# Performance work log

Measured on AMD Instinct MI355X. Metric: run time of the kernel, lower is better.

## Reference

```python
import jax, jax.numpy as jnp
import numpy as np

NEG_SLOPE = 0.01  # torch LeakyReLU default
VAR = 0.1


def _leaky(z):
    return jnp.where(z >= 0, z, NEG_SLOPE * z)


def _sconv(theta, bias, L, x):
    # theta: (C_out, C_in, 2), L: (M, M), x: (B, C_in, M)
    Lx = jnp.einsum('mn,bin->bim', L, x)                     # degree-1 Laplacian term
    y = jnp.einsum('oi,bim->bom', theta[:, :, 0], x) \
        + jnp.einsum('oi,bim->bom', theta[:, :, 1], Lx)
    if bias is not None:
        y = y + bias
    return y


def setup_inputs() -> dict:
    key = jax.random.key(0)
    ks = iter(jax.random.split(key, 32))
    B, Cin = 8, 4
    Ms = [2000, 6000, 4000]
    inp = {}
    for d, M in enumerate(Ms):
        inp[f'L{d}'] = jax.random.normal(next(ks), (M, M), jnp.float32) / np.sqrt(M)
        inp[f'x{d}'] = jax.random.normal(next(ks), (B, Cin, M), jnp.float32)
        inp[f'th{d}_1'] = VAR * jax.random.normal(next(ks), (16, 4, 2), jnp.float32)
        inp[f'b{d}_1'] = jnp.zeros((1, 16, 1), jnp.float32)
        inp[f'th{d}_2'] = VAR * jax.random.normal(next(ks), (32, 16, 2), jnp.float32)
    dims = [(96, 64), (64, 32), (32, 16), (16, 2)]
    for i, (din, dout) in enumerate(dims, start=1):
        bound = 1.0 / np.sqrt(din)
        inp[f'W{i}'] = jax.random.uniform(next(ks), (dout, din), jnp.float32, -bound, bound)
        inp[f'bb{i}'] = jax.random.uniform(next(ks), (dout,), jnp.float32, -bound, bound)
    return inp


def reference(L0, L1, L2, x0, x1, x2,
              th0_1, b0_1, th0_2,
              th1_1, b1_1, th1_2,
              th2_1, b2_1, th2_2,
              W1, bb1, W2, bb2, W3, bb3, W4, bb4):
    out0_1 = _sconv(th0_1, b0_1, L0, x0)
    out1_1 = _sconv(th1_1, b1_1, L1, x1)
    out2_1 = _sconv(th2_1, b2_1, L2, x2)
    out0_2 = _sconv(th0_2, None, L0, _leaky(out0_1))   # (B, 32, M0)
    out1_2 = _sconv(th1_2, None, L1, _leaky(out1_1))
    out2_2 = _sconv(th2_2, None, L2, _leaky(out2_1))
    # mean-pool over simplices, concat along channel dim -> (B, 96)
    pooled = jnp.concatenate([out0_2.mean(axis=2), out1_2.mean(axis=2), out2_2.mean(axis=2)], axis=1)
    h = pooled @ W1.T + bb1      # dropouts are identity at inference
    h = h @ W2.T + bb2
    h = h @ W3.T + bb3
    logits = h @ W4.T + bb4      # (B, 2)
    return (logits, out0_2, out1_2, out2_2)
```

## Files before the change

kernel.cpp:

```cpp
#include <hip/hip_runtime.h>
#include <stdint.h>

typedef __attribute__((ext_vector_type(4))) float f32x4;
typedef __attribute__((ext_vector_type(8))) __bf16 bf16x8;

constexpr int MS_[3] = {2000, 6000, 4000};
constexpr int MP_[3] = {2048, 6144, 4096};
constexpr int KS_[3] = {512, 1536, 1024};
constexpr int RB_[3] = {32, 96, 64};
constexpr int NB_[3] = {128, 384, 256};
constexpr int NTILE = 192;
constexpr int NGEMMB = 768;
constexpr long long OUT_OFF_[3] = {16, 512016, 2048016};

__device__ __forceinline__ unsigned short f2bf(float f) {
  __bf16 b = (__bf16)f;
  return *reinterpret_cast<unsigned short*>(&b);
}

__device__ __forceinline__ void gload_lds16(const void* g, void* l) {
  __builtin_amdgcn_global_load_lds(
      (const __attribute__((address_space(1))) unsigned int*)g,
      (__attribute__((address_space(3))) unsigned int*)l, 16, 0, 0);
}

template <int BN>
__device__ __forceinline__ void wait_main() {
  if constexpr (BN == 128) asm volatile("s_waitcnt vmcnt(12)" ::: "memory");
  else                     asm volatile("s_waitcnt vmcnt(6)" ::: "memory");
}
template <int BN>
__device__ __forceinline__ void wait_tail() {
  if constexpr (BN == 128) asm volatile("s_waitcnt vmcnt(8)" ::: "memory");
  else                     asm volatile("s_waitcnt vmcnt(5)" ::: "memory");
}
__device__ __forceinline__ void wait_zero() {
  asm volatile("s_waitcnt vmcnt(0)" ::: "memory");
}
__device__ __forceinline__ void bar_pin() {
  __builtin_amdgcn_s_barrier();
  __builtin_amdgcn_sched_barrier(0);
}

__device__ __forceinline__ void tile_decode(int bid, int& d, int& t) {
  if (bid < RB_[0]) { d = 0; t = bid; }
  else if (bid < RB_[0] + RB_[1]) { d = 1; t = bid - RB_[0]; }
  else { d = 2; t = bid - RB_[0] - RB_[1]; }
}

struct PrepArgs {
  const float* x[3];
  unsigned short* xT[3];
  float* zero0; int zero_n;
};

__global__ __launch_bounds__(256) void prep_k(PrepArgs pa) {
  int d, t; tile_decode(blockIdx.x, d, t);
  const int M = MS_[d], Mp = MP_[d];
  const float* x = pa.x[d];
  unsigned short* xT = pa.xT[d];
  const int tid = threadIdx.x;
  const int m0 = t * 64;
  const int ml = tid & 63, cg = tid >> 6;
  const int m = m0 + ml;
  const bool valid = m < M;
#pragma unroll
  for (int it = 0; it < 8; ++it) {
    int c = it * 4 + cg;
    float v = valid ? x[(size_t)c * M + m] : 0.f;
    xT[(size_t)c * Mp + m] = f2bf(v);
  }
  if (blockIdx.x == 0) {
    for (int i = tid; i < pa.zero_n; i += 256) pa.zero0[i] = 0.f;
  }
}

struct GemmArgs {
  const float* L[3];
  const unsigned short* B[3];
  float* P[3];
};

template <int BN>
__global__ __launch_bounds__(256, 2) void gemm_k(GemmArgs ga) {
  const int bid = blockIdx.x;
  int d, local;
  if (bid < NB_[1]) { d = 1; local = bid; }
  else if (bid < NB_[1] + NB_[2]) { d = 2; local = bid - NB_[1]; }
  else { d = 0; local = bid - NB_[1] - NB_[2]; }

  const int M = MS_[d], Mp = MP_[d], KS = KS_[d], RB = RB_[d];
  const int r = local % RB, s = local / RB;

  const float* __restrict__ Lp = ga.L[d];
  const unsigned short* __restrict__ Bt = ga.B[d];
  float* __restrict__ Pp = ga.P[d];

  const int m0 = r * 64;
  const int kt0 = s * KS;
  const int nsteps = KS >> 6;

  __shared__ __align__(16) unsigned short Bl[4][BN * 64];

  const int tid = threadIdx.x;
  const int lane = tid & 63;
  const int wave = tid >> 6;
  const int lr = lane & 15, lk = lane >> 4;
  constexpr int NR = BN / 16;
  constexpr int BI = BN / 32;

  int rowg = m0 + wave * 16 + lr;
  if (rowg > M - 1) rowg = M - 1;
  const float* __restrict__ pA = Lp + (size_t)rowg * M;

  const unsigned short* srcB[BI];
#pragma unroll
  for (int j = 0; j < BI; ++j) {
    int colg = (wave * BI + j) * 8 + (lane >> 3);
    int ke = ((lane & 7) * 8) ^ ((colg & 7) << 3);
    srcB[j] = Bt + (size_t)colg * Mp + ke;
  }

  f32x4 acc[NR];
#pragma unroll
  for (int n = 0; n < NR; ++n) acc[n] = (f32x4){0.f, 0.f, 0.f, 0.f};

  auto stageB = [&](int buf, int step) {
    const int kt = kt0 + step * 64;
#pragma unroll
    for (int j = 0; j < BI; ++j)
      gload_lds16(srcB[j] + kt, &Bl[buf][(wave * BI + j) * 512]);
  };
  auto loadA = [&](f32x4 (&ab)[2][2], int step) {
    const int kt = kt0 + step * 64;
#pragma unroll
    for (int kk = 0; kk < 2; ++kk) {
      int k = kt + kk * 32 + lk * 8;
      if (k + 8 > M) k = 0;
      const float* p = pA + k;
      ab[kk][0] = *reinterpret_cast<const f32x4*>(p);
      ab[kk][1] = *reinterpret_cast<const f32x4*>(p + 4);
    }
  };
  auto compute = [&](f32x4 (&ab)[2][2], int buf) {
    bf16x8 af[2];
#pragma unroll
    for (int kk = 0; kk < 2; ++kk)
#pragma unroll
      for (int j = 0; j < 4; ++j) {
        af[kk][j] = (__bf16)ab[kk][0][j];
        af[kk][4 + j] = (__bf16)ab[kk][1][j];
      }
    const unsigned short* Bb = &Bl[buf][0];
#pragma unroll
    for (int nr = 0; nr < NR; ++nr) {
      const int col = nr * 16 + lr;
      const int base = col * 64, swz = (col & 7) << 3;
      bf16x8 b0 = *reinterpret_cast<const bf16x8*>(&Bb[base + ((lk * 8) ^ swz)]);
      bf16x8 b1 = *reinterpret_cast<const bf16x8*>(&Bb[base + ((32 + lk * 8) ^ swz)]);
      acc[nr] = __builtin_amdgcn_mfma_f32_16x16x32_bf16(af[0], b0, acc[nr], 0, 0, 0);
      acc[nr] = __builtin_amdgcn_mfma_f32_16x16x32_bf16(af[1], b1, acc[nr], 0, 0, 0);
    }
  };

  f32x4 a0[2][2], a1[2][2];
  stageB(0, 0);
  loadA(a0, 0);
  stageB(1, 1);

  for (int t = 0; t < nsteps - 2; t += 2) {
    loadA(a1, t + 1);
    stageB((t + 2) & 3, t + 2);
    wait_main<BN>();
    bar_pin();
    compute(a0, t & 3);
    loadA(a0, t + 2);
    stageB((t + 3) & 3, t + 3);
    wait_main<BN>();
    bar_pin();
    compute(a1, (t + 1) & 3);
  }
  loadA(a1, nsteps - 1);
  wait_tail<BN>();
  bar_pin();
  compute(a0, (nsteps - 2) & 3);
  wait_zero();
  bar_pin();
  compute(a1, (nsteps - 1) & 3);

  const int rowb = m0 + wave * 16 + lk * 4;
#pragma unroll
  for (int nr = 0; nr < NR; ++nr) {
    const int cc = nr * 16 + lr;
#pragma unroll
    for (int j = 0; j < 4; ++j) {
      int rr = rowb + j;
      Pp[((size_t)s * Mp + rr) * BN + cc] = acc[nr][j];
    }
  }
}

struct EpiAArgs {
  const float* part1[3];
  const float* x[3];
  const float* th1[3];
  const float* b1[3];
  unsigned short* zT[3];
};

__global__ __launch_bounds__(256) void epiA_k(EpiAArgs ea) {
  int d, t; tile_decode(blockIdx.x, d, t);
  const int M = MS_[d], Mp = MP_[d];
  const int m0 = t * 64;
  __shared__ float Ys[32 * 66];
  __shared__ float Xs[32 * 66];
  const int tid = threadIdx.x;
  const float* part = ea.part1[d];
#pragma unroll
  for (int it = 0; it < 8; ++it) {
    int idx = it * 256 + tid;
    int m = idx >> 5, c = idx & 31;
    size_t base = (size_t)(m0 + m) * 32 + c;
    size_t st = (size_t)Mp * 32;
    float ssum = part[base] + part[st + base] + part[2 * st + base] + part[3 * st + base];
    Ys[c * 66 + m] = ssum;
  }
  {
    const float* x = ea.x[d];
    int m = tid & 63, cg = tid >> 6;
    bool valid = (m0 + m) < M;
#pragma unroll
    for (int it = 0; it < 8; ++it) {
      int c = it * 4 + cg;
      Xs[c * 66 + m] = valid ? x[(size_t)c * M + m0 + m] : 0.f;
    }
  }
  __syncthreads();
  const float* th = ea.th1[d];
  const float* bias = ea.b1[d];
  unsigned short* zT = ea.zT[d];
  const int m = tid & 63, cog = tid >> 6;
  const bool valid = (m0 + m) < M;
#pragma unroll
  for (int it = 0; it < 32; ++it) {
    int co = it * 4 + cog;
    int o = co & 15, b = co >> 4;
    float a = bias[o];
#pragma unroll
    for (int i = 0; i < 4; ++i) {
      int ci = b * 4 + i;
      a += th[(o * 4 + i) * 2] * Xs[ci * 66 + m] + th[(o * 4 + i) * 2 + 1] * Ys[ci * 66 + m];
    }
    float zz = (a >= 0.f) ? a : 0.01f * a;
    zT[(size_t)co * Mp + m0 + m] = valid ? f2bf(zz) : (unsigned short)0;
  }
}

struct EpiBArgs {
  const float* part2[3];
  const unsigned short* zT[3];
  const float* th2[3];
  float* out;
  float* csz;
  float* csy;
};

__global__ __launch_bounds__(256) void epiB_k(EpiBArgs eb) {
  int d, t; tile_decode(blockIdx.x, d, t);
  const int M = MS_[d], Mp = MP_[d];
  const int m0 = t * 64;
  __shared__ float Ys[128 * 66];
  __shared__ float red[256];
  const int tid = threadIdx.x;
  const float* part = eb.part2[d];
  float csum = 0.f;
#pragma unroll
  for (int it = 0; it < 32; ++it) {
    int idx = it * 256 + tid;
    int m = idx >> 7, c = idx & 127;
    size_t base = (size_t)(m0 + m) * 128 + c;
    size_t st = (size_t)Mp * 128;
    float ssum = part[base] + part[st + base] + part[2 * st + base] + part[3 * st + base];
    Ys[c * 66 + m] = ssum;
    if (m0 + m < M) csum += ssum;
  }
  red[tid] = csum;
  __syncthreads();
  if (tid < 128) atomicAdd(&eb.csy[d * 128 + tid], red[tid] + red[tid + 128]);

  const unsigned short* zT = eb.zT[d];
  const float* th = eb.th2[d];
  float* outp = eb.out + OUT_OFF_[d];
  const int m = tid & 63, g = tid >> 6;
  const bool valid = (m0 + m) < M;
#pragma unroll
  for (int bb = 0; bb < 2; ++bb) {
    int b = g * 2 + bb;
    float zv[16], yv[16];
#pragma unroll
    for (int o1 = 0; o1 < 16; ++o1) {
      int c = b * 16 + o1;
      unsigned short raw = zT[(size_t)c * Mp + m0 + m];
      __bf16 bf = *reinterpret_cast<__bf16*>(&raw);
      zv[o1] = (float)bf;
      yv[o1] = Ys[c * 66 + m];
    }
#pragma unroll
    for (int o1 = 0; o1 < 16; ++o1) {
      float v = zv[o1];
#pragma unroll
      for (int off = 32; off > 0; off >>= 1) v += __shfl_xor(v, off, 64);
      if (m == 0) atomicAdd(&eb.csz[d * 128 + b * 16 + o1], v);
    }
#pragma unroll
    for (int o2 = 0; o2 < 32; ++o2) {
      float v = 0.f;
#pragma unroll
      for (int o1 = 0; o1 < 16; ++o1)
        v += th[(o2 * 16 + o1) * 2] * zv[o1] + th[(o2 * 16 + o1) * 2 + 1] * yv[o1];
      if (valid) outp[(size_t)(b * 32 + o2) * M + m0 + m] = v;
    }
  }
}

struct MlpArgs {
  const float* csz; const float* csy;
  const float* th2[3];
  const float* W1; const float* b1;
  const float* W2; const float* b2;
  const float* W3; const float* b3;
  const float* W4; const float* b4;
  float* out;
};

__global__ __launch_bounds__(256) void mlp_k(MlpArgs ma) {
  __shared__ float pl[8][96];
  __shared__ float h1[8][64];
  __shared__ float h2[8][32];
  __shared__ float h3[8][16];
  const int tid = threadIdx.x;
  for (int id = tid; id < 768; id += 256) {
    int d = id >> 8, rem = id & 255, b = rem >> 5, o2 = rem & 31;
    const float* th = ma.th2[d];
    float invM = 1.f / (float)MS_[d];
    float v = 0.f;
    for (int o1 = 0; o1 < 16; ++o1)
      v += th[(o2 * 16 + o1) * 2] * ma.csz[d * 128 + b * 16 + o1] +
           th[(o2 * 16 + o1) * 2 + 1] * ma.csy[d * 128 + b * 16 + o1];
    pl[b][d * 32 + o2] = v * invM;
  }
  __syncthreads();
  for (int id = tid; id < 512; id += 256) {
    int b = id >> 6, j = id & 63;
    float v = ma.b1[j];
    for (int k = 0; k < 96; ++k) v += pl[b][k] * ma.W1[j * 96 + k];
    h1[b][j] = v;
  }
  __syncthreads();
  {
    int b = tid >> 5, j = tid & 31;
    float v = ma.b2[j];
    for (int k = 0; k < 64; ++k) v += h1[b][k] * ma.W2[j * 64 + k];
    h2[b][j] = v;
  }
  __syncthreads();
  if (tid < 128) {
    int b = tid >> 4, j = tid & 15;
    float v = ma.b3[j];
    for (int k = 0; k < 32; ++k) v += h2[b][k] * ma.W3[j * 32 + k];
    h3[b][j] = v;
  }
  __syncthreads();
  if (tid < 16) {
    int b = tid >> 1, j = tid & 1;
    float v = ma.b4[j];
    for (int k = 0; k < 16; ++k) v += h3[b][k] * ma.W4[j * 16 + k];
    ma.out[tid] = v;
  }
}

extern "C" void kernel_launch(void* const* d_in, const int* in_sizes, int n_in,
                              void* d_out, int out_size, void* d_ws, size_t ws_size,
                              hipStream_t stream) {
  (void)in_sizes; (void)n_in; (void)out_size; (void)ws_size;
  const float* L[3]   = {(const float*)d_in[0], (const float*)d_in[5], (const float*)d_in[10]};
  const float* x[3]   = {(const float*)d_in[1], (const float*)d_in[6], (const float*)d_in[11]};
  const float* th1[3] = {(const float*)d_in[2], (const float*)d_in[7], (const float*)d_in[12]};
  const float* b1[3]  = {(const float*)d_in[3], (const float*)d_in[8], (const float*)d_in[13]};
  const float* th2[3] = {(const float*)d_in[4], (const float*)d_in[9], (const float*)d_in[14]};
  const float* W1 = (const float*)d_in[15]; const float* bb1 = (const float*)d_in[16];
  const float* W2 = (const float*)d_in[17]; const float* bb2 = (const float*)d_in[18];
  const float* W3 = (const float*)d_in[19]; const float* bb3 = (const float*)d_in[20];
  const float* W4 = (const float*)d_in[21]; const float* bb4 = (const float*)d_in[22];
  float* out = (float*)d_out;

  char* ws = (char*)d_ws;
  size_t off = 0;
  auto alloc = [&](size_t bytes) {
    size_t r = off;
    off = (off + bytes + 255) & ~(size_t)255;
    return r;
  };
  const int MPs[3] = {2048, 6144, 4096};
  unsigned short* xT[3]; unsigned short* zT[3]; float* p1[3]; float* p2[3];
  for (int d = 0; d < 3; ++d) xT[d] = (unsigned short*)(ws + alloc((size_t)32 * MPs[d] * 2));
  for (int d = 0; d < 3; ++d) zT[d] = (unsigned short*)(ws + alloc((size_t)128 * MPs[d] * 2));
  for (int d = 0; d < 3; ++d) p1[d] = (float*)(ws + alloc((size_t)4 * MPs[d] * 32 * 4));
  for (int d = 0; d < 3; ++d) p2[d] = (float*)(ws + alloc((size_t)4 * MPs[d] * 128 * 4));
  float* csz = (float*)(ws + alloc((size_t)3 * 128 * 4));
  float* csy = (float*)(ws + alloc((size_t)3 * 128 * 4));

  PrepArgs pa;
  for (int d = 0; d < 3; ++d) { pa.x[d] = x[d]; pa.xT[d] = xT[d]; }
  pa.zero0 = csz; pa.zero_n = 768;
  prep_k<<<NTILE, 256, 0, stream>>>(pa);

  GemmArgs g1;
  for (int d = 0; d < 3; ++d) { g1.L[d] = L[d]; g1.B[d] = xT[d]; g1.P[d] = p1[d]; }
  gemm_k<32><<<NGEMMB, 256, 0, stream>>>(g1);

  EpiAArgs ea;
  for (int d = 0; d < 3; ++d) {
    ea.part1[d] = p1[d]; ea.x[d] = x[d]; ea.th1[d] = th1[d]; ea.b1[d] = b1[d]; ea.zT[d] = zT[d];
  }
  epiA_k<<<NTILE, 256, 0, stream>>>(ea);

  GemmArgs g2;
  for (int d = 0; d < 3; ++d) { g2.L[d] = L[d]; g2.B[d] = zT[d]; g2.P[d] = p2[d]; }
  gemm_k<128><<<NGEMMB, 256, 0, stream>>>(g2);

  EpiBArgs eb;
  for (int d = 0; d < 3; ++d) { eb.part2[d] = p2[d]; eb.zT[d] = zT[d]; eb.th2[d] = th2[d]; }
  eb.out = out; eb.csz = csz; eb.csy = csy;
  epiB_k<<<NTILE, 256, 0, stream>>>(eb);

  MlpArgs ma;
  ma.csz = csz; ma.csy = csy;
  for (int d = 0; d < 3; ++d) ma.th2[d] = th2[d];
  ma.W1 = W1; ma.b1 = bb1; ma.W2 = W2; ma.b2 = bb2;
  ma.W3 = W3; ma.b3 = bb3; ma.W4 = W4; ma.b4 = bb4;
  ma.out = out;
  mlp_k<<<1, 256, 0, stream>>>(ma);
}
```

Baseline: 187.5 us.

## Split GEMM into specialised kernels with wider split-K and retuned pipelines

The shared templated GEMM becomes two kernels. gemm1 (N=32) uses 128-row tiles with two M-fragments per wave and 16-way split-K, giving 1536 blocks at occupancy 4. gemm2 (N=128) moves to a 3-slot LDS ring at occupancy 3. Both get a unified steady-state loop with clamped prefetch in place of explicit tail handling. The goal is more parallelism and better latency hiding for the memory-bound L streaming of the first GEMM, at the cost of a 16-way partial reduction in epiA and a shared partial buffer reused by both stages.

```diff
diff --git a/kernel.cpp b/kernel.cpp
--- a/kernel.cpp
+++ b/kernel.cpp
@@ -6,11 +6,16 @@
 
 constexpr int MS_[3] = {2000, 6000, 4000};
 constexpr int MP_[3] = {2048, 6144, 4096};
-constexpr int KS_[3] = {512, 1536, 1024};
 constexpr int RB_[3] = {32, 96, 64};
-constexpr int NB_[3] = {128, 384, 256};
 constexpr int NTILE = 192;
-constexpr int NGEMMB = 768;
+constexpr int RBB1_[3] = {16, 48, 32};
+constexpr int NB1_[3] = {256, 768, 512};
+constexpr int NG1 = 1536;
+constexpr int KS1_[3] = {128, 384, 256};
+constexpr int RB2_[3] = {32, 96, 64};
+constexpr int NB2_[3] = {128, 384, 256};
+constexpr int NG2 = 768;
+constexpr int KS2_[3] = {512, 1536, 1024};
 constexpr long long OUT_OFF_[3] = {16, 512016, 2048016};
 
 __device__ __forceinline__ unsigned short f2bf(float f) {
@@ -24,19 +29,6 @@
       (__attribute__((address_space(3))) unsigned int*)l, 16, 0, 0);
 }
 
-template <int BN>
-__device__ __forceinline__ void wait_main() {
-  if constexpr (BN == 128) asm volatile("s_waitcnt vmcnt(12)" ::: "memory");
-  else                     asm volatile("s_waitcnt vmcnt(6)" ::: "memory");
-}
-template <int BN>
-__device__ __forceinline__ void wait_tail() {
-  if constexpr (BN == 128) asm volatile("s_waitcnt vmcnt(8)" ::: "memory");
-  else                     asm volatile("s_waitcnt vmcnt(5)" ::: "memory");
-}
-__device__ __forceinline__ void wait_zero() {
-  asm volatile("s_waitcnt vmcnt(0)" ::: "memory");
-}
 __device__ __forceinline__ void bar_pin() {
   __builtin_amdgcn_s_barrier();
   __builtin_amdgcn_sched_barrier(0);
@@ -75,61 +67,182 @@
   }
 }
 
-struct GemmArgs {
+struct G1Args {
   const float* L[3];
   const unsigned short* B[3];
   float* P[3];
 };
 
-template <int BN>
-__global__ __launch_bounds__(256, 2) void gemm_k(GemmArgs ga) {
+__global__ __launch_bounds__(256, 4) void gemm1_k(G1Args ga) {
   const int bid = blockIdx.x;
   int d, local;
-  if (bid < NB_[1]) { d = 1; local = bid; }
-  else if (bid < NB_[1] + NB_[2]) { d = 2; local = bid - NB_[1]; }
-  else { d = 0; local = bid - NB_[1] - NB_[2]; }
-
-  const int M = MS_[d], Mp = MP_[d], KS = KS_[d], RB = RB_[d];
+  if (bid < NB1_[1]) { d = 1; local = bid; }
+  else if (bid < NB1_[1] + NB1_[2]) { d = 2; local = bid - NB1_[1]; }
+  else { d = 0; local = bid - NB1_[1] - NB1_[2]; }
+
+  const int M = MS_[d], Mp = MP_[d], KS = KS1_[d], RB = RBB1_[d];
   const int r = local % RB, s = local / RB;
-
   const float* __restrict__ Lp = ga.L[d];
   const unsigned short* __restrict__ Bt = ga.B[d];
   float* __restrict__ Pp = ga.P[d];
 
-  const int m0 = r * 64;
+  const int m0 = r * 128;
   const int kt0 = s * KS;
-  const int nsteps = KS >> 6;
-
-  __shared__ __align__(16) unsigned short Bl[4][BN * 64];
+  const int ns = KS >> 6;
+
+  __shared__ __align__(16) unsigned short Bl[4][32 * 64];
 
   const int tid = threadIdx.x;
   const int lane = tid & 63;
   const int wave = tid >> 6;
   const int lr = lane & 15, lk = lane >> 4;
-  constexpr int NR = BN / 16;
-  constexpr int BI = BN / 32;
+
+  const float* pA[2];
+#pragma unroll
+  for (int mr = 0; mr < 2; ++mr) {
+    int row = m0 + wave * 32 + mr * 16 + lr;
+    if (row > M - 1) row = M - 1;
+    pA[mr] = Lp + (size_t)row * M;
+  }
+  const int colg = tid >> 3;
+  const int ke = ((tid & 7) * 8) ^ ((colg & 7) << 3);
+  const unsigned short* srcB = Bt + (size_t)colg * Mp + ke;
+
+  f32x4 acc[2][2];
+#pragma unroll
+  for (int a = 0; a < 2; ++a)
+#pragma unroll
+    for (int b = 0; b < 2; ++b) acc[a][b] = (f32x4){0.f, 0.f, 0.f, 0.f};
+
+  auto mstep = [&](int x) { return x < ns ? x : ns - 1; };
+  auto stageB = [&](int slot, int step) {
+    gload_lds16(srcB + kt0 + step * 64, &Bl[slot][tid * 8]);
+  };
+  auto loadA = [&](f32x4 (&ab)[2][2][2], int step) {
+    const int kt = kt0 + step * 64;
+#pragma unroll
+    for (int mr = 0; mr < 2; ++mr)
+#pragma unroll
+      for (int kk = 0; kk < 2; ++kk) {
+        int k = kt + kk * 32 + lk * 8;
+        if (k + 8 > M) k = 0;
+        const float* p = pA[mr] + k;
+        ab[mr][kk][0] = *reinterpret_cast<const f32x4*>(p);
+        ab[mr][kk][1] = *reinterpret_cast<const f32x4*>(p + 4);
+      }
+  };
+  auto compute = [&](f32x4 (&ab)[2][2][2], int slot) {
+    bf16x8 af[2][2];
+#pragma unroll
+    for (int mr = 0; mr < 2; ++mr)
+#pragma unroll
+      for (int kk = 0; kk < 2; ++kk)
+#pragma unroll
+        for (int j = 0; j < 4; ++j) {
+          af[mr][kk][j] = (__bf16)ab[mr][kk][0][j];
+          af[mr][kk][4 + j] = (__bf16)ab[mr][kk][1][j];
+        }
+    const unsigned short* Bb = &Bl[slot][0];
+#pragma unroll
+    for (int nr = 0; nr < 2; ++nr) {
+      const int col = nr * 16 + lr;
+      const int base = col * 64, swz = (col & 7) << 3;
+      bf16x8 b0 = *reinterpret_cast<const bf16x8*>(&Bb[base + ((lk * 8) ^ swz)]);
+      bf16x8 b1 = *reinterpret_cast<const bf16x8*>(&Bb[base + ((32 + lk * 8) ^ swz)]);
+#pragma unroll
+      for (int mr = 0; mr < 2; ++mr) {
+        acc[mr][nr] = __builtin_amdgcn_mfma_f32_16x16x32_bf16(af[mr][0], b0, acc[mr][nr], 0, 0, 0);
+        acc[mr][nr] = __builtin_amdgcn_mfma_f32_16x16x32_bf16(af[mr][1], b1, acc[mr][nr], 0, 0, 0);
+      }
+    }
+  };
+
+  f32x4 a0[2][2][2], a1[2][2][2];
+  stageB(0, 0);
+  stageB(2, mstep(2));
+  loadA(a0, 0);
+  stageB(1, mstep(1));
+  loadA(a1, mstep(1));
+
+  for (int t = 0; t < ns; t += 2) {
+    asm volatile("s_waitcnt vmcnt(9)" ::: "memory");
+    bar_pin();
+    stageB((t + 3) & 3, mstep(t + 3));
+    compute(a0, t & 3);
+    loadA(a0, mstep(t + 2));
+
+    asm volatile("s_waitcnt vmcnt(9)" ::: "memory");
+    bar_pin();
+    stageB((t + 4) & 3, mstep(t + 4));
+    compute(a1, (t + 1) & 3);
+    loadA(a1, mstep(t + 3));
+  }
+
+#pragma unroll
+  for (int mr = 0; mr < 2; ++mr) {
+    const int rowb = m0 + wave * 32 + mr * 16 + lk * 4;
+#pragma unroll
+    for (int nr = 0; nr < 2; ++nr) {
+      const int cc = nr * 16 + lr;
+#pragma unroll
+      for (int j = 0; j < 4; ++j)
+        Pp[((size_t)s * Mp + rowb + j) * 32 + cc] = acc[mr][nr][j];
+    }
+  }
+}
+
+struct G2Args {
+  const float* L[3];
+  const unsigned short* B[3];
+  float* P[3];
+};
+
+__global__ __launch_bounds__(256, 3) void gemm2_k(G2Args ga) {
+  const int bid = blockIdx.x;
+  int d, local;
+  if (bid < NB2_[1]) { d = 1; local = bid; }
+  else if (bid < NB2_[1] + NB2_[2]) { d = 2; local = bid - NB2_[1]; }
+  else { d = 0; local = bid - NB2_[1] - NB2_[2]; }
+
+  const int M = MS_[d], Mp = MP_[d], KS = KS2_[d], RB = RB2_[d];
+  const int r = local % RB, s = local / RB;
+  const float* __restrict__ Lp = ga.L[d];
+  const unsigned short* __restrict__ Bt = ga.B[d];
+  float* __restrict__ Pp = ga.P[d];
+
+  const int m0 = r * 64;
+  const int kt0 = s * KS;
+  const int ns = KS >> 6;
+
+  __shared__ __align__(16) unsigned short Bl[3][128 * 64];
+
+  const int tid = threadIdx.x;
+  const int lane = tid & 63;
+  const int wave = tid >> 6;
+  const int lr = lane & 15, lk = lane >> 4;
 
   int rowg = m0 + wave * 16 + lr;
   if (rowg > M - 1) rowg = M - 1;
   const float* __restrict__ pA = Lp + (size_t)rowg * M;
 
-  const unsigned short* srcB[BI];
-#pragma unroll
-  for (int j = 0; j < BI; ++j) {
-    int colg = (wave * BI + j) * 8 + (lane >> 3);
-    int ke = ((lane & 7) * 8) ^ ((colg & 7) << 3);
-    srcB[j] = Bt + (size_t)colg * Mp + ke;
-  }
-
-  f32x4 acc[NR];
-#pragma unroll
-  for (int n = 0; n < NR; ++n) acc[n] = (f32x4){0.f, 0.f, 0.f, 0.f};
-
-  auto stageB = [&](int buf, int step) {
+  const unsigned short* srcB[4];
+#pragma unroll
+  for (int j = 0; j < 4; ++j) {
+    int colg = (wave * 4 + j) * 8 + (lane >> 3);
+    int ke2 = ((lane & 7) * 8) ^ ((colg & 7) << 3);
+    srcB[j] = Bt + (size_t)colg * Mp + ke2;
+  }
+
+  f32x4 acc[8];
+#pragma unroll
+  for (int n = 0; n < 8; ++n) acc[n] = (f32x4){0.f, 0.f, 0.f, 0.f};
+
+  auto mstep = [&](int x) { return x < ns ? x : ns - 1; };
+  auto stageB = [&](int slot, int step) {
     const int kt = kt0 + step * 64;
 #pragma unroll
-    for (int j = 0; j < BI; ++j)
-      gload_lds16(srcB[j] + kt, &Bl[buf][(wave * BI + j) * 512]);
+    for (int j = 0; j < 4; ++j)
+      gload_lds16(srcB[j] + kt, &Bl[slot][(wave * 4 + j) * 512 + lane * 8]);
   };
   auto loadA = [&](f32x4 (&ab)[2][2], int step) {
     const int kt = kt0 + step * 64;
@@ -142,7 +255,7 @@
       ab[kk][1] = *reinterpret_cast<const f32x4*>(p + 4);
     }
   };
-  auto compute = [&](f32x4 (&ab)[2][2], int buf) {
+  auto compute = [&](f32x4 (&ab)[2][2], int slot) {
     bf16x8 af[2];
 #pragma unroll
     for (int kk = 0; kk < 2; ++kk)
@@ -151,9 +264,9 @@
         af[kk][j] = (__bf16)ab[kk][0][j];
         af[kk][4 + j] = (__bf16)ab[kk][1][j];
       }
-    const unsigned short* Bb = &Bl[buf][0];
-#pragma unroll
-    for (int nr = 0; nr < NR; ++nr) {
+    const unsigned short* Bb = &Bl[slot][0];
+#pragma unroll
+    for (int nr = 0; nr < 8; ++nr) {
       const int col = nr * 16 + lr;
       const int base = col * 64, swz = (col & 7) << 3;
       bf16x8 b0 = *reinterpret_cast<const bf16x8*>(&Bb[base + ((lk * 8) ^ swz)]);
@@ -166,37 +279,30 @@
   f32x4 a0[2][2], a1[2][2];
   stageB(0, 0);
   loadA(a0, 0);
-  stageB(1, 1);
-
-  for (int t = 0; t < nsteps - 2; t += 2) {
-    loadA(a1, t + 1);
-    stageB((t + 2) & 3, t + 2);
-    wait_main<BN>();
+  stageB(1, mstep(1));
+  loadA(a1, mstep(1));
+
+  for (int t = 0; t < ns; t += 2) {
+    asm volatile("s_waitcnt vmcnt(8)" ::: "memory");
     bar_pin();
-    compute(a0, t & 3);
-    loadA(a0, t + 2);
-    stageB((t + 3) & 3, t + 3);
-    wait_main<BN>();
+    stageB((t + 2) % 3, mstep(t + 2));
+    compute(a0, t % 3);
+    loadA(a0, mstep(t + 2));
+
+    asm volatile("s_waitcnt vmcnt(8)" ::: "memory");
     bar_pin();
-    compute(a1, (t + 1) & 3);
-  }
-  loadA(a1, nsteps - 1);
-  wait_tail<BN>();
-  bar_pin();
-  compute(a0, (nsteps - 2) & 3);
-  wait_zero();
-  bar_pin();
-  compute(a1, (nsteps - 1) & 3);
+    stageB((t + 3) % 3, mstep(t + 3));
+    compute(a1, (t + 1) % 3);
+    loadA(a1, mstep(t + 3));
+  }
 
   const int rowb = m0 + wave * 16 + lk * 4;
 #pragma unroll
-  for (int nr = 0; nr < NR; ++nr) {
+  for (int nr = 0; nr < 8; ++nr) {
     const int cc = nr * 16 + lr;
 #pragma unroll
-    for (int j = 0; j < 4; ++j) {
-      int rr = rowb + j;
-      Pp[((size_t)s * Mp + rr) * BN + cc] = acc[nr][j];
-    }
+    for (int j = 0; j < 4; ++j)
+      Pp[((size_t)s * Mp + rowb + j) * 128 + cc] = acc[nr][j];
   }
 }
 
@@ -216,13 +322,15 @@
   __shared__ float Xs[32 * 66];
   const int tid = threadIdx.x;
   const float* part = ea.part1[d];
+  const size_t st = (size_t)Mp * 32;
 #pragma unroll
   for (int it = 0; it < 8; ++it) {
     int idx = it * 256 + tid;
     int m = idx >> 5, c = idx & 31;
     size_t base = (size_t)(m0 + m) * 32 + c;
-    size_t st = (size_t)Mp * 32;
-    float ssum = part[base] + part[st + base] + part[2 * st + base] + part[3 * st + base];
+    float ssum = 0.f;
+#pragma unroll
+    for (int s5 = 0; s5 < 16; ++s5) ssum += part[s5 * st + base];
     Ys[c * 66 + m] = ssum;
   }
   {
@@ -402,11 +510,10 @@
     return r;
   };
   const int MPs[3] = {2048, 6144, 4096};
-  unsigned short* xT[3]; unsigned short* zT[3]; float* p1[3]; float* p2[3];
+  unsigned short* xT[3]; unsigned short* zT[3]; float* pb[3];
   for (int d = 0; d < 3; ++d) xT[d] = (unsigned short*)(ws + alloc((size_t)32 * MPs[d] * 2));
   for (int d = 0; d < 3; ++d) zT[d] = (unsigned short*)(ws + alloc((size_t)128 * MPs[d] * 2));
-  for (int d = 0; d < 3; ++d) p1[d] = (float*)(ws + alloc((size_t)4 * MPs[d] * 32 * 4));
-  for (int d = 0; d < 3; ++d) p2[d] = (float*)(ws + alloc((size_t)4 * MPs[d] * 128 * 4));
+  for (int d = 0; d < 3; ++d) pb[d] = (float*)(ws + alloc((size_t)16 * MPs[d] * 32 * 4));
   float* csz = (float*)(ws + alloc((size_t)3 * 128 * 4));
   float* csy = (float*)(ws + alloc((size_t)3 * 128 * 4));
 
@@ -415,22 +522,22 @@
   pa.zero0 = csz; pa.zero_n = 768;
   prep_k<<<NTILE, 256, 0, stream>>>(pa);
 
-  GemmArgs g1;
-  for (int d = 0; d < 3; ++d) { g1.L[d] = L[d]; g1.B[d] = xT[d]; g1.P[d] = p1[d]; }
-  gemm_k<32><<<NGEMMB, 256, 0, stream>>>(g1);
+  G1Args g1;
+  for (int d = 0; d < 3; ++d) { g1.L[d] = L[d]; g1.B[d] = xT[d]; g1.P[d] = pb[d]; }
+  gemm1_k<<<NG1, 256, 0, stream>>>(g1);
 
   EpiAArgs ea;
   for (int d = 0; d < 3; ++d) {
-    ea.part1[d] = p1[d]; ea.x[d] = x[d]; ea.th1[d] = th1[d]; ea.b1[d] = b1[d]; ea.zT[d] = zT[d];
+    ea.part1[d] = pb[d]; ea.x[d] = x[d]; ea.th1[d] = th1[d]; ea.b1[d] = b1[d]; ea.zT[d] = zT[d];
   }
   epiA_k<<<NTILE, 256, 0, stream>>>(ea);
 
-  GemmArgs g2;
-  for (int d = 0; d < 3; ++d) { g2.L[d] = L[d]; g2.B[d] = zT[d]; g2.P[d] = p2[d]; }
-  gemm_k<128><<<NGEMMB, 256, 0, stream>>>(g2);
+  G2Args g2;
+  for (int d = 0; d < 3; ++d) { g2.L[d] = L[d]; g2.B[d] = zT[d]; g2.P[d] = pb[d]; }
+  gemm2_k<<<NG2, 256, 0, stream>>>(g2);
 
   EpiBArgs eb;
-  for (int d = 0; d < 3; ++d) { eb.part2[d] = p2[d]; eb.zT[d] = zT[d]; eb.th2[d] = th2[d]; }
+  for (int d = 0; d < 3; ++d) { eb.part2[d] = pb[d]; eb.zT[d] = zT[d]; eb.th2[d] = th2[d]; }
   eb.out = out; eb.csz = csz; eb.csy = csy;
   epiB_k<<<NTILE, 256, 0, stream>>>(eb);
 
```

Measured after the change: 190.6 us. About the same (+1.6%).

## Stage L tiles through LDS ring, raise split-K for pass 1, split N for pass 2

Applied to the files above, without the earlier changes.

Both GEMM passes now load the fp32 L tile asynchronously into a swizzled LDS ring with global_load_lds instead of into registers, and use a single-step ring pipeline with a fixed vmcnt wait. Pass 1 uses a much larger split-K (8-16 splits) to get more blocks in flight. Pass 2 splits the 128 output columns into two 64-wide halves, doubling the blocks. This targets latency hiding and occupancy on the memory-bound L stream, at the cost of reading L twice in pass 2, more partial sums for epiA to reduce, and a shared partial buffer reused between passes.

```diff
diff --git a/kernel.cpp b/kernel.cpp
--- a/kernel.cpp
+++ b/kernel.cpp
@@ -6,12 +6,15 @@
 
 constexpr int MS_[3] = {2000, 6000, 4000};
 constexpr int MP_[3] = {2048, 6144, 4096};
-constexpr int KS_[3] = {512, 1536, 1024};
 constexpr int RB_[3] = {32, 96, 64};
-constexpr int NB_[3] = {128, 384, 256};
 constexpr int NTILE = 192;
-constexpr int NGEMMB = 768;
 constexpr long long OUT_OFF_[3] = {16, 512016, 2048016};
+
+constexpr int S1_[3] = {8, 16, 16};
+constexpr int KS1_[3] = {256, 384, 256};
+constexpr int NG1 = 1536 + 1024 + 256;
+constexpr int KS2_[3] = {512, 1536, 1024};
+constexpr int NG2 = 768 + 512 + 256;
 
 __device__ __forceinline__ unsigned short f2bf(float f) {
   __bf16 b = (__bf16)f;
@@ -24,19 +27,6 @@
       (__attribute__((address_space(3))) unsigned int*)l, 16, 0, 0);
 }
 
-template <int BN>
-__device__ __forceinline__ void wait_main() {
-  if constexpr (BN == 128) asm volatile("s_waitcnt vmcnt(12)" ::: "memory");
-  else                     asm volatile("s_waitcnt vmcnt(6)" ::: "memory");
-}
-template <int BN>
-__device__ __forceinline__ void wait_tail() {
-  if constexpr (BN == 128) asm volatile("s_waitcnt vmcnt(8)" ::: "memory");
-  else                     asm volatile("s_waitcnt vmcnt(5)" ::: "memory");
-}
-__device__ __forceinline__ void wait_zero() {
-  asm volatile("s_waitcnt vmcnt(0)" ::: "memory");
-}
 __device__ __forceinline__ void bar_pin() {
   __builtin_amdgcn_s_barrier();
   __builtin_amdgcn_sched_barrier(0);
@@ -75,22 +65,33 @@
   }
 }
 
-struct GemmArgs {
+struct GArgs {
   const float* L[3];
   const unsigned short* B[3];
   float* P[3];
 };
 
-template <int BN>
-__global__ __launch_bounds__(256, 2) void gemm_k(GemmArgs ga) {
-  const int bid = blockIdx.x;
-  int d, local;
-  if (bid < NB_[1]) { d = 1; local = bid; }
-  else if (bid < NB_[1] + NB_[2]) { d = 2; local = bid - NB_[1]; }
-  else { d = 0; local = bid - NB_[1] - NB_[2]; }
-
-  const int M = MS_[d], Mp = MP_[d], KS = KS_[d], RB = RB_[d];
-  const int r = local % RB, s = local / RB;
+template <int PASS>
+__global__ __launch_bounds__(256, 2) void gemm_k(GArgs ga) {
+  int bid = blockIdx.x;
+  int d, r, s, nh = 0;
+  if constexpr (PASS == 1) {
+    if (bid < 1536) { d = 1; r = bid % 96; s = bid / 96; }
+    else if (bid < 2560) { bid -= 1536; d = 2; r = bid % 64; s = bid / 64; }
+    else { bid -= 2560; d = 0; r = bid % 32; s = bid / 32; }
+  } else {
+    if (bid < 768) { d = 1; r = bid % 96; int q = bid / 96; nh = q & 1; s = q >> 1; }
+    else if (bid < 1280) { bid -= 768; d = 2; r = bid % 64; int q = bid / 64; nh = q & 1; s = q >> 1; }
+    else { bid -= 1280; d = 0; r = bid % 32; int q = bid / 32; nh = q & 1; s = q >> 1; }
+  }
+  const int M = MS_[d], Mp = MP_[d];
+  const int KS = (PASS == 1) ? KS1_[d] : KS2_[d];
+  const int ns = KS >> 6;
+  constexpr int BN = (PASS == 1) ? 32 : 64;
+  constexpr int PW = (PASS == 1) ? 32 : 128;
+  constexpr int RING = (PASS == 1) ? 4 : 3;
+  constexpr int NR = BN / 16;
+  constexpr int BI = BN / 32;
 
   const float* __restrict__ Lp = ga.L[d];
   const unsigned short* __restrict__ Bt = ga.B[d];
@@ -98,105 +99,101 @@
 
   const int m0 = r * 64;
   const int kt0 = s * KS;
-  const int nsteps = KS >> 6;
-
-  __shared__ __align__(16) unsigned short Bl[4][BN * 64];
+
+  __shared__ __align__(16) char Al[RING][64 * 256];
+  __shared__ __align__(16) char Bl[RING][BN * 128];
 
   const int tid = threadIdx.x;
   const int lane = tid & 63;
   const int wave = tid >> 6;
   const int lr = lane & 15, lk = lane >> 4;
-  constexpr int NR = BN / 16;
-  constexpr int BI = BN / 32;
-
-  int rowg = m0 + wave * 16 + lr;
-  if (rowg > M - 1) rowg = M - 1;
-  const float* __restrict__ pA = Lp + (size_t)rowg * M;
-
+
+  const float* pAsrc[4];
+  int koffA[4];
+#pragma unroll
+  for (int j = 0; j < 4; ++j) {
+    int ldsb = j * 4096 + tid * 16;
+    int row = ldsb >> 8;
+    int inner = (ldsb & 255) ^ ((row & 7) << 5);
+    int grow = m0 + row;
+    if (grow > M - 1) grow = M - 1;
+    pAsrc[j] = Lp + (size_t)grow * M;
+    koffA[j] = inner >> 2;
+  }
   const unsigned short* srcB[BI];
 #pragma unroll
   for (int j = 0; j < BI; ++j) {
-    int colg = (wave * BI + j) * 8 + (lane >> 3);
-    int ke = ((lane & 7) * 8) ^ ((colg & 7) << 3);
-    srcB[j] = Bt + (size_t)colg * Mp + ke;
+    int ldsb = j * 4096 + tid * 16;
+    int col = ldsb >> 7;
+    int inner = (ldsb & 127) ^ ((col & 7) << 4);
+    srcB[j] = Bt + (size_t)(nh * 64 + col) * Mp + (inner >> 1);
   }
 
   f32x4 acc[NR];
 #pragma unroll
   for (int n = 0; n < NR; ++n) acc[n] = (f32x4){0.f, 0.f, 0.f, 0.f};
 
-  auto stageB = [&](int buf, int step) {
+  auto mstep = [&](int x) { return x < ns ? x : ns - 1; };
+  auto stage = [&](int slot, int step) {
     const int kt = kt0 + step * 64;
 #pragma unroll
+    for (int j = 0; j < 4; ++j) {
+      int gk = kt + koffA[j];
+      if (gk + 4 > M) gk = 0;
+      gload_lds16(pAsrc[j] + gk, &Al[slot][j * 4096 + tid * 16]);
+    }
+#pragma unroll
     for (int j = 0; j < BI; ++j)
-      gload_lds16(srcB[j] + kt, &Bl[buf][(wave * BI + j) * 512]);
+      gload_lds16(srcB[j] + kt, &Bl[slot][j * 4096 + tid * 16]);
   };
-  auto loadA = [&](f32x4 (&ab)[2][2], int step) {
-    const int kt = kt0 + step * 64;
+  auto compute = [&](int slot) {
+    const char* Ab = &Al[slot][0];
+    const char* Bb = &Bl[slot][0];
+    const int rowl = wave * 16 + lr;
+    const int abase = rowl * 256;
+    const int aswz = (rowl & 7) << 5;
+    bf16x8 af[2];
 #pragma unroll
     for (int kk = 0; kk < 2; ++kk) {
-      int k = kt + kk * 32 + lk * 8;
-      if (k + 8 > M) k = 0;
-      const float* p = pA + k;
-      ab[kk][0] = *reinterpret_cast<const f32x4*>(p);
-      ab[kk][1] = *reinterpret_cast<const f32x4*>(p + 4);
-    }
-  };
-  auto compute = [&](f32x4 (&ab)[2][2], int buf) {
-    bf16x8 af[2];
-#pragma unroll
-    for (int kk = 0; kk < 2; ++kk)
+      int off = abase + ((kk * 128 + lk * 32) ^ aswz);
+      f32x4 v0 = *reinterpret_cast<const f32x4*>(Ab + off);
+      f32x4 v1 = *reinterpret_cast<const f32x4*>(Ab + off + 16);
 #pragma unroll
       for (int j = 0; j < 4; ++j) {
-        af[kk][j] = (__bf16)ab[kk][0][j];
-        af[kk][4 + j] = (__bf16)ab[kk][1][j];
+        af[kk][j] = (__bf16)v0[j];
+        af[kk][4 + j] = (__bf16)v1[j];
       }
-    const unsigned short* Bb = &Bl[buf][0];
+    }
 #pragma unroll
     for (int nr = 0; nr < NR; ++nr) {
       const int col = nr * 16 + lr;
-      const int base = col * 64, swz = (col & 7) << 3;
-      bf16x8 b0 = *reinterpret_cast<const bf16x8*>(&Bb[base + ((lk * 8) ^ swz)]);
-      bf16x8 b1 = *reinterpret_cast<const bf16x8*>(&Bb[base + ((32 + lk * 8) ^ swz)]);
+      const int bbase = col * 128, bswz = (col & 7) << 4;
+      bf16x8 b0 = *reinterpret_cast<const bf16x8*>(Bb + bbase + ((lk * 16) ^ bswz));
+      bf16x8 b1 = *reinterpret_cast<const bf16x8*>(Bb + bbase + ((64 + lk * 16) ^ bswz));
       acc[nr] = __builtin_amdgcn_mfma_f32_16x16x32_bf16(af[0], b0, acc[nr], 0, 0, 0);
       acc[nr] = __builtin_amdgcn_mfma_f32_16x16x32_bf16(af[1], b1, acc[nr], 0, 0, 0);
     }
   };
 
-  f32x4 a0[2][2], a1[2][2];
-  stageB(0, 0);
-  loadA(a0, 0);
-  stageB(1, 1);
-
-  for (int t = 0; t < nsteps - 2; t += 2) {
-    loadA(a1, t + 1);
-    stageB((t + 2) & 3, t + 2);
-    wait_main<BN>();
+  stage(0, 0);
+  stage(1, mstep(1));
+  if constexpr (RING == 4) stage(2, mstep(2));
+
+  for (int t = 0; t < ns; ++t) {
+    if constexpr (PASS == 1) asm volatile("s_waitcnt vmcnt(10)" ::: "memory");
+    else                     asm volatile("s_waitcnt vmcnt(6)" ::: "memory");
     bar_pin();
-    compute(a0, t & 3);
-    loadA(a0, t + 2);
-    stageB((t + 3) & 3, t + 3);
-    wait_main<BN>();
-    bar_pin();
-    compute(a1, (t + 1) & 3);
-  }
-  loadA(a1, nsteps - 1);
-  wait_tail<BN>();
-  bar_pin();
-  compute(a0, (nsteps - 2) & 3);
-  wait_zero();
-  bar_pin();
-  compute(a1, (nsteps - 1) & 3);
+    stage((t + RING - 1) % RING, mstep(t + RING - 1));
+    compute(t % RING);
+  }
 
   const int rowb = m0 + wave * 16 + lk * 4;
 #pragma unroll
   for (int nr = 0; nr < NR; ++nr) {
-    const int cc = nr * 16 + lr;
-#pragma unroll
-    for (int j = 0; j < 4; ++j) {
-      int rr = rowb + j;
-      Pp[((size_t)s * Mp + rr) * BN + cc] = acc[nr][j];
-    }
+    const int cc = (PASS == 1 ? 0 : nh * 64) + nr * 16 + lr;
+#pragma unroll
+    for (int j = 0; j < 4; ++j)
+      Pp[((size_t)s * Mp + rowb + j) * PW + cc] = acc[nr][j];
   }
 }
 
@@ -216,13 +213,15 @@
   __shared__ float Xs[32 * 66];
   const int tid = threadIdx.x;
   const float* part = ea.part1[d];
+  const size_t st = (size_t)Mp * 32;
+  const int S1 = S1_[d];
 #pragma unroll
   for (int it = 0; it < 8; ++it) {
     int idx = it * 256 + tid;
     int m = idx >> 5, c = idx & 31;
     size_t base = (size_t)(m0 + m) * 32 + c;
-    size_t st = (size_t)Mp * 32;
-    float ssum = part[base] + part[st + base] + part[2 * st + base] + part[3 * st + base];
+    float ssum = 0.f;
+    for (int s5 = 0; s5 < S1; ++s5) ssum += part[s5 * st + base];
     Ys[c * 66 + m] = ssum;
   }
   {
@@ -402,11 +401,10 @@
     return r;
   };
   const int MPs[3] = {2048, 6144, 4096};
-  unsigned short* xT[3]; unsigned short* zT[3]; float* p1[3]; float* p2[3];
+  unsigned short* xT[3]; unsigned short* zT[3]; float* pb[3];
   for (int d = 0; d < 3; ++d) xT[d] = (unsigned short*)(ws + alloc((size_t)32 * MPs[d] * 2));
   for (int d = 0; d < 3; ++d) zT[d] = (unsigned short*)(ws + alloc((size_t)128 * MPs[d] * 2));
-  for (int d = 0; d < 3; ++d) p1[d] = (float*)(ws + alloc((size_t)4 * MPs[d] * 32 * 4));
-  for (int d = 0; d < 3; ++d) p2[d] = (float*)(ws + alloc((size_t)4 * MPs[d] * 128 * 4));
+  for (int d = 0; d < 3; ++d) pb[d] = (float*)(ws + alloc((size_t)16 * MPs[d] * 32 * 4));
   float* csz = (float*)(ws + alloc((size_t)3 * 128 * 4));
   float* csy = (float*)(ws + alloc((size_t)3 * 128 * 4));
 
@@ -415,22 +413,22 @@
   pa.zero0 = csz; pa.zero_n = 768;
   prep_k<<<NTILE, 256, 0, stream>>>(pa);
 
-  GemmArgs g1;
-  for (int d = 0; d < 3; ++d) { g1.L[d] = L[d]; g1.B[d] = xT[d]; g1.P[d] = p1[d]; }
-  gemm_k<32><<<NGEMMB, 256, 0, stream>>>(g1);
+  GArgs g1;
+  for (int d = 0; d < 3; ++d) { g1.L[d] = L[d]; g1.B[d] = xT[d]; g1.P[d] = pb[d]; }
+  gemm_k<1><<<NG1, 256, 0, stream>>>(g1);
 
   EpiAArgs ea;
   for (int d = 0; d < 3; ++d) {
-    ea.part1[d] = p1[d]; ea.x[d] = x[d]; ea.th1[d] = th1[d]; ea.b1[d] = b1[d]; ea.zT[d] = zT[d];
+    ea.part1[d] = pb[d]; ea.x[d] = x[d]; ea.th1[d] = th1[d]; ea.b1[d] = b1[d]; ea.zT[d] = zT[d];
   }
   epiA_k<<<NTILE, 256, 0, stream>>>(ea);
 
-  GemmArgs g2;
-  for (int d = 0; d < 3; ++d) { g2.L[d] = L[d]; g2.B[d] = zT[d]; g2.P[d] = p2[d]; }
-  gemm_k<128><<<NGEMMB, 256, 0, stream>>>(g2);
+  GArgs g2;
+  for (int d = 0; d < 3; ++d) { g2.L[d] = L[d]; g2.B[d] = zT[d]; g2.P[d] = pb[d]; }
+  gemm_k<2><<<NG2, 256, 0, stream>>>(g2);
 
   EpiBArgs eb;
-  for (int d = 0; d < 3; ++d) { eb.part2[d] = p2[d]; eb.zT[d] = zT[d]; eb.th2[d] = th2[d]; }
+  for (int d = 0; d < 3; ++d) { eb.part2[d] = pb[d]; eb.zT[d] = zT[d]; eb.th2[d] = th2[d]; }
   eb.out = out; eb.csz = csz; eb.csy = csy;
   epiB_k<<<NTILE, 256, 0, stream>>>(eb);
 
```

Result: slower. 226.1 us (+20.6%).

## Double split-K for first GEMM, add XCD block swizzle, share partial buffer

Applied to the files above, without the earlier changes.

The first Laplacian GEMM (32 columns) now splits K into 8 slices instead of 4, doubling its grid to 1536 blocks so more CUs are busy on this skinny GEMM. Both GEMMs remap block IDs so that consecutive blocks land on the same XCD, aiming for better L2 reuse of L and B tiles. The A-register prefetch is moved to the end of each loop iteration, and the two partial buffers are merged into one shared workspace. In exchange, the epilogue must reduce 8 partial slices and more partial traffic is written to memory.

```diff
diff --git a/kernel.cpp b/kernel.cpp
--- a/kernel.cpp
+++ b/kernel.cpp
@@ -6,12 +6,16 @@
 
 constexpr int MS_[3] = {2000, 6000, 4000};
 constexpr int MP_[3] = {2048, 6144, 4096};
-constexpr int KS_[3] = {512, 1536, 1024};
 constexpr int RB_[3] = {32, 96, 64};
-constexpr int NB_[3] = {128, 384, 256};
 constexpr int NTILE = 192;
-constexpr int NGEMMB = 768;
 constexpr long long OUT_OFF_[3] = {16, 512016, 2048016};
+
+constexpr int KS1_[3] = {256, 768, 512};
+constexpr int NB1_[3] = {256, 768, 512};
+constexpr int NG1 = 1536;
+constexpr int KS2_[3] = {512, 1536, 1024};
+constexpr int NB2_[3] = {128, 384, 256};
+constexpr int NG2 = 768;
 
 __device__ __forceinline__ unsigned short f2bf(float f) {
   __bf16 b = (__bf16)f;
@@ -40,6 +44,11 @@
 __device__ __forceinline__ void bar_pin() {
   __builtin_amdgcn_s_barrier();
   __builtin_amdgcn_sched_barrier(0);
+}
+
+__device__ __forceinline__ int xcd_swz(int bid, int nwg) {
+  int cpx = nwg >> 3;
+  return (bid & 7) * cpx + (bid >> 3);
 }
 
 __device__ __forceinline__ void tile_decode(int bid, int& d, int& t) {
@@ -83,13 +92,20 @@
 
 template <int BN>
 __global__ __launch_bounds__(256, 2) void gemm_k(GemmArgs ga) {
-  const int bid = blockIdx.x;
+  int bid = xcd_swz(blockIdx.x, (BN == 32) ? NG1 : NG2);
   int d, local;
-  if (bid < NB_[1]) { d = 1; local = bid; }
-  else if (bid < NB_[1] + NB_[2]) { d = 2; local = bid - NB_[1]; }
-  else { d = 0; local = bid - NB_[1] - NB_[2]; }
-
-  const int M = MS_[d], Mp = MP_[d], KS = KS_[d], RB = RB_[d];
+  if constexpr (BN == 32) {
+    if (bid < NB1_[1]) { d = 1; local = bid; }
+    else if (bid < NB1_[1] + NB1_[2]) { d = 2; local = bid - NB1_[1]; }
+    else { d = 0; local = bid - NB1_[1] - NB1_[2]; }
+  } else {
+    if (bid < NB2_[1]) { d = 1; local = bid; }
+    else if (bid < NB2_[1] + NB2_[2]) { d = 2; local = bid - NB2_[1]; }
+    else { d = 0; local = bid - NB2_[1] - NB2_[2]; }
+  }
+
+  const int M = MS_[d], Mp = MP_[d], RB = RB_[d];
+  const int KS = (BN == 32) ? KS1_[d] : KS2_[d];
   const int r = local % RB, s = local / RB;
 
   const float* __restrict__ Lp = ga.L[d];
@@ -167,9 +183,9 @@
   stageB(0, 0);
   loadA(a0, 0);
   stageB(1, 1);
+  loadA(a1, 1);
 
   for (int t = 0; t < nsteps - 2; t += 2) {
-    loadA(a1, t + 1);
     stageB((t + 2) & 3, t + 2);
     wait_main<BN>();
     bar_pin();
@@ -179,8 +195,8 @@
     wait_main<BN>();
     bar_pin();
     compute(a1, (t + 1) & 3);
-  }
-  loadA(a1, nsteps - 1);
+    loadA(a1, t + 3);
+  }
   wait_tail<BN>();
   bar_pin();
   compute(a0, (nsteps - 2) & 3);
@@ -216,13 +232,15 @@
   __shared__ float Xs[32 * 66];
   const int tid = threadIdx.x;
   const float* part = ea.part1[d];
+  const size_t st = (size_t)Mp * 32;
 #pragma unroll
   for (int it = 0; it < 8; ++it) {
     int idx = it * 256 + tid;
     int m = idx >> 5, c = idx & 31;
     size_t base = (size_t)(m0 + m) * 32 + c;
-    size_t st = (size_t)Mp * 32;
-    float ssum = part[base] + part[st + base] + part[2 * st + base] + part[3 * st + base];
+    float ssum = 0.f;
+#pragma unroll
+    for (int s5 = 0; s5 < 8; ++s5) ssum += part[s5 * st + base];
     Ys[c * 66 + m] = ssum;
   }
   {
@@ -402,11 +420,10 @@
     return r;
   };
   const int MPs[3] = {2048, 6144, 4096};
-  unsigned short* xT[3]; unsigned short* zT[3]; float* p1[3]; float* p2[3];
+  unsigned short* xT[3]; unsigned short* zT[3]; float* pb[3];
   for (int d = 0; d < 3; ++d) xT[d] = (unsigned short*)(ws + alloc((size_t)32 * MPs[d] * 2));
   for (int d = 0; d < 3; ++d) zT[d] = (unsigned short*)(ws + alloc((size_t)128 * MPs[d] * 2));
-  for (int d = 0; d < 3; ++d) p1[d] = (float*)(ws + alloc((size_t)4 * MPs[d] * 32 * 4));
-  for (int d = 0; d < 3; ++d) p2[d] = (float*)(ws + alloc((size_t)4 * MPs[d] * 128 * 4));
+  for (int d = 0; d < 3; ++d) pb[d] = (float*)(ws + alloc((size_t)MPs[d] * 2048));
   float* csz = (float*)(ws + alloc((size_t)3 * 128 * 4));
   float* csy = (float*)(ws + alloc((size_t)3 * 128 * 4));
 
@@ -416,21 +433,21 @@
   prep_k<<<NTILE, 256, 0, stream>>>(pa);
 
   GemmArgs g1;
-  for (int d = 0; d < 3; ++d) { g1.L[d] = L[d]; g1.B[d] = xT[d]; g1.P[d] = p1[d]; }
-  gemm_k<32><<<NGEMMB, 256, 0, stream>>>(g1);
+  for (int d = 0; d < 3; ++d) { g1.L[d] = L[d]; g1.B[d] = xT[d]; g1.P[d] = pb[d]; }
+  gemm_k<32><<<NG1, 256, 0, stream>>>(g1);
 
   EpiAArgs ea;
   for (int d = 0; d < 3; ++d) {
-    ea.part1[d] = p1[d]; ea.x[d] = x[d]; ea.th1[d] = th1[d]; ea.b1[d] = b1[d]; ea.zT[d] = zT[d];
+    ea.part1[d] = pb[d]; ea.x[d] = x[d]; ea.th1[d] = th1[d]; ea.b1[d] = b1[d]; ea.zT[d] = zT[d];
   }
   epiA_k<<<NTILE, 256, 0, stream>>>(ea);
 
   GemmArgs g2;
-  for (int d = 0; d < 3; ++d) { g2.L[d] = L[d]; g2.B[d] = zT[d]; g2.P[d] = p2[d]; }
-  gemm_k<128><<<NGEMMB, 256, 0, stream>>>(g2);
+  for (int d = 0; d < 3; ++d) { g2.L[d] = L[d]; g2.B[d] = zT[d]; g2.P[d] = pb[d]; }
+  gemm_k<128><<<NG2, 256, 0, stream>>>(g2);
 
   EpiBArgs eb;
-  for (int d = 0; d < 3; ++d) { eb.part2[d] = p2[d]; eb.zT[d] = zT[d]; eb.th2[d] = th2[d]; }
+  for (int d = 0; d < 3; ++d) { eb.part2[d] = pb[d]; eb.zT[d] = zT[d]; eb.th2[d] = th2[d]; }
   eb.out = out; eb.csz = csz; eb.csy = csy;
   epiB_k<<<NTILE, 256, 0, stream>>>(eb);
 
```

Result: slower. 192.8 us (+2.8%).
